# Kernel optimization log

Hardware: AMD Instinct MI355X
Metric: run time of the kernel (lower is better)

Reference implementation:

```python
import jax, jax.numpy as jnp
import numpy as np

D_MODEL = 2048
N_HEADS = 16
D_HEAD = D_MODEL // N_HEADS
B, T, CACHE_LEN = 2, 2048, 2048


def setup_inputs() -> dict:
    key = jax.random.key(0)
    k1, k2, k3, k4, k5 = jax.random.split(key, 5)
    s = 0.02
    return {
        "x": jax.random.normal(k1, (B, T, D_MODEL), dtype=jnp.float32),
        "Wqkv": jax.random.normal(k2, (3 * D_MODEL, D_MODEL), dtype=jnp.float32) * s,
        "Wproj": jax.random.normal(k3, (D_MODEL, D_MODEL), dtype=jnp.float32) * s,
        "cache_k": jax.random.normal(k4, (B, N_HEADS, CACHE_LEN, D_HEAD), dtype=jnp.float32),
        "cache_v": jax.random.normal(k5, (B, N_HEADS, CACHE_LEN, D_HEAD), dtype=jnp.float32),
    }


def reference(x, Wqkv, Wproj, cache_k, cache_v):
    b, t, c = x.shape
    h, d = N_HEADS, D_HEAD
    scale = d ** -0.5
    # qkv projection (torch Linear: x @ W.T), split into q,k,v
    qkv = jnp.einsum('btc,fc->btf', x, Wqkv)
    q, k, v = jnp.split(qkv, 3, axis=-1)
    # [b, t, c] -> [b, h, t, d]
    q = q.reshape(b, t, h, d).transpose(0, 2, 1, 3)
    k = k.reshape(b, t, h, d).transpose(0, 2, 1, 3)
    v = v.reshape(b, t, h, d).transpose(0, 2, 1, 3)
    cache_len = cache_k.shape[2]
    k = jnp.concatenate([cache_k, k], axis=2)  # [b, h, kv_len, d]
    v = jnp.concatenate([cache_v, v], axis=2)
    kv_len = k.shape[2]
    scores = jnp.einsum('bhtd,bhsd->bhts', q, k) * scale
    # causal mask with cache offset: key_pos <= query_pos
    query_pos = jnp.arange(t) + cache_len
    key_pos = jnp.arange(kv_len)
    mask = key_pos[None, :] <= query_pos[:, None]  # [t, kv_len]
    neg = jnp.finfo(scores.dtype).min
    scores = jnp.where(mask[None, None, :, :], scores, neg)
    attn = jax.nn.softmax(scores, axis=-1)
    y = jnp.einsum('bhts,bhsd->bhtd', attn, v)
    y = y.transpose(0, 2, 1, 3).reshape(b, t, c)
    return jnp.einsum('btc,oc->bto', y, Wproj)
```

## Files before the change

### kernel.cpp

```cpp
#include <hip/hip_runtime.h>

#define B_ 2
#define T_ 2048
#define H_ 16
#define D_ 128
#define DM_ 2048
#define CL_ 2048
#define KV_ 4096

typedef __attribute__((ext_vector_type(8))) short short8;
typedef __attribute__((ext_vector_type(4))) float f32x4;
typedef __attribute__((ext_vector_type(16))) float f32x16;
typedef unsigned short u16;

__device__ __forceinline__ u16 f2bf(float f) {
    unsigned u = __float_as_uint(f);
    u += 0x7FFFu + ((u >> 16) & 1u);
    return (u16)(u >> 16);
}

__device__ __forceinline__ void gload16(const void* g, void* l) {
    __builtin_amdgcn_global_load_lds((__attribute__((address_space(1))) const void*)g,
                                     (__attribute__((address_space(3))) void*)l, 16, 0, 0);
}


__global__ void cvt4(const float* __restrict__ src, u16* __restrict__ dst, int n4) {
    int i = blockIdx.x * 256 + threadIdx.x;
    if (i >= n4) return;
    const float4 v = *(const float4*)(src + (long)i * 4);
    ushort4 o;
    o.x = f2bf(v.x); o.y = f2bf(v.y); o.z = f2bf(v.z); o.w = f2bf(v.w);
    *(ushort4*)(dst + (long)i * 4) = o;
}

__global__ void cvt_cachek(const float* __restrict__ ck, u16* __restrict__ Kc) {
    int i = blockIdx.x * 256 + threadIdx.x;
    int kc = i & 15, s = (i >> 4) & 2047, bh = i >> 15;
    const float* src = ck + ((long)bh * 2048 + s) * 128 + kc * 8;
    float4 v0 = *(const float4*)src, v1 = *(const float4*)(src + 4);
    short8 o;
    o[0] = f2bf(v0.x); o[1] = f2bf(v0.y); o[2] = f2bf(v0.z); o[3] = f2bf(v0.w);
    o[4] = f2bf(v1.x); o[5] = f2bf(v1.y); o[6] = f2bf(v1.z); o[7] = f2bf(v1.w);
    *(short8*)(Kc + ((long)(bh * 16 + kc) * 4096 + s) * 8) = o;
}

__global__ void cvt_cachev(const float* __restrict__ cv, u16* __restrict__ Vc) {
    int i = blockIdx.x * 256 + threadIdx.x;
    int d = i & 127, ch = (i >> 7) & 255, bh = i >> 15;
    const float* src = cv + ((long)bh * 2048 + ch * 8) * 128 + d;
    short8 o;
#pragma unroll
    for (int j = 0; j < 8; ++j) o[j] = f2bf(src[j * 128]);
    *(short8*)(Vc + ((long)(bh * 512 + ch) * 128 + d) * 8) = o;
}


template <int MODE>
__global__ void gemm_bt(const u16* __restrict__ A, const u16* __restrict__ Bt,
                        int K,
                        u16* __restrict__ Qb, u16* __restrict__ Kc,
                        u16* __restrict__ Vc, float* __restrict__ Out) {
    __shared__ __align__(16) char A_lds[128 * 128];
    __shared__ __align__(16) char B_lds[128 * 128];

    const int tid = threadIdx.x;
    const int w = tid >> 6, l = tid & 63;
    const int wm = w >> 1, wn = w & 1;
    const int lg = l >> 4, lc = l & 15;
    const long m0 = (long)blockIdx.y * 128, n0 = (long)blockIdx.x * 128;

    f32x4 acc[4][4] = {};

    const char* Ab = (const char*)A + m0 * (K * 2);
    const char* Bb = (const char*)Bt + n0 * (K * 2);

    for (int k0 = 0; k0 < K; k0 += 64) {
#pragma unroll
        for (int j = 0; j < 4; ++j) {
            int o = ((w * 4 + j) << 10) + l * 16;
            int row = o >> 7, col = o & 127;
            gload16(Ab + (long)row * (K * 2) + k0 * 2 + col, A_lds + ((w * 4 + j) << 10));
            gload16(Bb + (long)row * (K * 2) + k0 * 2 + col, B_lds + ((w * 4 + j) << 10));
        }
        __syncthreads();
#pragma unroll
        for (int kk = 0; kk < 64; kk += 32) {
            short8 a[4], b[4];
#pragma unroll
            for (int f = 0; f < 4; ++f) {
                a[f] = *(const short8*)(A_lds + (wm * 64 + f * 16 + lc) * 128 + (kk + lg * 8) * 2);
                b[f] = *(const short8*)(B_lds + (wn * 64 + f * 16 + lc) * 128 + (kk + lg * 8) * 2);
            }
#pragma unroll
            for (int mf = 0; mf < 4; ++mf)
#pragma unroll
                for (int nf = 0; nf < 4; ++nf)
                    acc[mf][nf] = __builtin_amdgcn_mfma_f32_16x16x32_bf16(a[mf], b[nf], acc[mf][nf], 0, 0, 0);
        }
        __syncthreads();
    }

    const float qscale = 0.088388347648318447f;
#pragma unroll
    for (int mf = 0; mf < 4; ++mf) {
#pragma unroll
        for (int nf = 0; nf < 4; ++nf) {
            int mbase = (int)m0 + wm * 64 + mf * 16 + lg * 4;
            int n = (int)n0 + wn * 64 + nf * 16 + lc;
#pragma unroll
            for (int r = 0; r < 4; ++r) {
                float c = acc[mf][nf][r];
                int m = mbase + r;
                if (MODE == 0) {
                    int b = m >> 11, t = m & 2047;
                    int sec = n >> 11, f = n & 2047;
                    int h = f >> 7, d = f & 127;
                    long bh = b * H_ + h;
                    int s = CL_ + t;
                    if (sec == 0)      Qb[(bh * T_ + t) * D_ + d] = f2bf(c * qscale);
                    else if (sec == 1) Kc[((bh * 16 + (d >> 3)) * 4096L + s) * 8 + (d & 7)] = f2bf(c);
                    else               Vc[((bh * 512 + (s >> 3)) * 128L + d) * 8 + (s & 7)] = f2bf(c);
                } else {
                    Out[(long)m * DM_ + n] = c;
                }
            }
        }
    }
}


__global__ __launch_bounds__(256, 2) void attn_fwd(const u16* __restrict__ Qb,
                                                   const u16* __restrict__ Kc,
                                                   const u16* __restrict__ Vc,
                                                   u16* __restrict__ Yb) {
    __shared__ __align__(16) char Klds[2][16384];

    const int tid = threadIdx.x;
    const int w = tid >> 6, l = tid & 63;
    const int col = l & 31, half = l >> 5;
    const int blk = blockIdx.x;
    const int xcd = blk & 7, ii = blk >> 3;
    const int bh = xcd * 4 + ((ii >> 4) & 1) + (((ii >> 5) & 1) << 1);
    const int q0 = ((ii & 32) ? (15 - (ii & 15)) : (ii & 15)) << 7;
    const int qw0 = q0 + w * 32;

    const char* kcb = (const char*)Kc + (long)bh * 1048576;
    const char* vcb = (const char*)Vc + (long)bh * 1048576;

    short8 qf[8];
    const u16* qp = Qb + ((long)bh * T_ + qw0 + col) * D_ + half * 8;
#pragma unroll
    for (int kmf = 0; kmf < 8; ++kmf) qf[kmf] = *(const short8*)(qp + kmf * 16);

    f32x16 oa[4] = {};
    float mrun = -1e38f, lrun = 0.f;

    auto stageK = [&](int s0, int b) {
#pragma unroll
        for (int j = 0; j < 4; ++j) {
            int kc = w * 4 + j;
            gload16(kcb + (long)kc * 65536 + (long)(s0 + l) * 16, Klds[b] + kc * 1024);
        }
    };

    stageK(0, 0);
    __syncthreads();

    const int sLast = q0 + 2112;
    int cur = 0;
    for (int s0 = 0; s0 <= sLast; s0 += 64) {
        const bool active = (s0 <= qw0 + 31 + CL_);

        short8 vf[16];
        if (active) {
            const char* vsrc = vcb + (long)s0 * 256;
#pragma unroll
            for (int db = 0; db < 4; ++db)
#pragma unroll
                for (int smf = 0; smf < 4; ++smf)
                    vf[db * 4 + smf] =
                        *(const short8*)(vsrc + (((smf * 2 + half) * 128 + db * 32 + col) << 4));
        }

        if (s0 < sLast) stageK(s0 + 64, cur ^ 1);

        if (active) {
            f32x16 p0 = {}, p1 = {};
#pragma unroll
            for (int kmf = 0; kmf < 8; ++kmf) {
                const char* kbase = Klds[cur] + (((kmf * 2 + half) * 64 + col) << 4);
                short8 kf0 = *(const short8*)(kbase);
                short8 kf1 = *(const short8*)(kbase + (32 << 4));
                p0 = __builtin_amdgcn_mfma_f32_32x32x16_bf16(kf0, qf[kmf], p0, 0, 0, 0);
                p1 = __builtin_amdgcn_mfma_f32_32x32x16_bf16(kf1, qf[kmf], p1, 0, 0, 0);
            }

            if (s0 + 63 > qw0 + CL_) {
                int qg = qw0 + col + CL_;
#pragma unroll
                for (int r = 0; r < 16; ++r) {
                    int sl = s0 + (r & 3) + 8 * (r >> 2) + 4 * half;
                    if (sl > qg)      p0[r] = -3e38f;
                    if (sl + 32 > qg) p1[r] = -3e38f;
                }
            }

            float m8[8];
#pragma unroll
            for (int i = 0; i < 8; ++i)
                m8[i] = fmaxf(fmaxf(p0[i], p0[i + 8]), fmaxf(p1[i], p1[i + 8]));
            float pmax = fmaxf(fmaxf(fmaxf(m8[0], m8[1]), fmaxf(m8[2], m8[3])),
                               fmaxf(fmaxf(m8[4], m8[5]), fmaxf(m8[6], m8[7])));
            pmax = fmaxf(pmax, __shfl_xor(pmax, 32));

            if (!__all(pmax - mrun <= 0.0f)) {
                float mnew = fmaxf(mrun, pmax);
                float scl = __expf(mrun - mnew);
                mrun = mnew;
                lrun *= scl;
                float sc[16];
#pragma unroll
                for (int r = 0; r < 16; ++r) sc[r] = __shfl(scl, (r & 3) + 8 * (r >> 2) + 4 * half);
#pragma unroll
                for (int db = 0; db < 4; ++db)
#pragma unroll
                    for (int r = 0; r < 16; ++r) oa[db][r] *= sc[r];
            }

#pragma unroll
            for (int r = 0; r < 16; ++r) {
                p0[r] = __expf(p0[r] - mrun);
                p1[r] = __expf(p1[r] - mrun);
            }
            float s8[8];
#pragma unroll
            for (int i = 0; i < 8; ++i) s8[i] = (p0[i] + p0[i + 8]) + (p1[i] + p1[i + 8]);
            float ts = ((s8[0] + s8[1]) + (s8[2] + s8[3])) + ((s8[4] + s8[5]) + (s8[6] + s8[7]));
            lrun += ts + __shfl_xor(ts, 32);

            short8 pa[4];
#pragma unroll
            for (int smf = 0; smf < 4; ++smf) {
                const f32x16& pp = (smf < 2) ? p0 : p1;
                const int r0 = (smf & 1) * 8;
                unsigned Alo = (unsigned)f2bf(pp[r0 + 0]) | ((unsigned)f2bf(pp[r0 + 1]) << 16);
                unsigned Ahi = (unsigned)f2bf(pp[r0 + 2]) | ((unsigned)f2bf(pp[r0 + 3]) << 16);
                unsigned Blo = (unsigned)f2bf(pp[r0 + 4]) | ((unsigned)f2bf(pp[r0 + 5]) << 16);
                unsigned Bhi = (unsigned)f2bf(pp[r0 + 6]) | ((unsigned)f2bf(pp[r0 + 7]) << 16);
                unsigned sAlo = __shfl_xor(Alo, 32), sAhi = __shfl_xor(Ahi, 32);
                unsigned sBlo = __shfl_xor(Blo, 32), sBhi = __shfl_xor(Bhi, 32);
                union { unsigned u[4]; short8 s; } U;
                if (half == 0) { U.u[0] = Alo;  U.u[1] = Ahi;  U.u[2] = sAlo; U.u[3] = sAhi; }
                else           { U.u[0] = sBlo; U.u[1] = sBhi; U.u[2] = Blo;  U.u[3] = Bhi; }
                pa[smf] = U.s;
            }

#pragma unroll
            for (int db = 0; db < 4; ++db) {
#pragma unroll
                for (int smf = 0; smf < 4; ++smf)
                    oa[db] = __builtin_amdgcn_mfma_f32_32x32x16_bf16(pa[smf], vf[db * 4 + smf], oa[db], 0, 0, 0);
            }
        }

        __syncthreads();
        cur ^= 1;
    }

    float inv = 1.0f / lrun;
    float li[16];
#pragma unroll
    for (int r = 0; r < 16; ++r) li[r] = __shfl(inv, (r & 3) + 8 * (r >> 2) + 4 * half);

    const int b = bh >> 4, h = bh & 15;
#pragma unroll
    for (int db = 0; db < 4; ++db)
#pragma unroll
        for (int r = 0; r < 16; ++r) {
            int t = qw0 + (r & 3) + 8 * (r >> 2) + 4 * half;
            Yb[((long)b * T_ + t) * DM_ + h * 128 + db * 32 + col] = f2bf(oa[db][r] * li[r]);
        }
}


extern "C" void kernel_launch(void* const* d_in, const int* in_sizes, int n_in,
                              void* d_out, int out_size, void* d_ws, size_t ws_size,
                              hipStream_t stream) {
    const float* x    = (const float*)d_in[0];
    const float* Wqkv = (const float*)d_in[1];
    const float* Wpr  = (const float*)d_in[2];
    const float* cK   = (const float*)d_in[3];
    const float* cV   = (const float*)d_in[4];
    float* out = (float*)d_out;

    char* p = (char*)d_ws;
    auto take = [&](long elems) { u16* r = (u16*)p; p += ((elems * 2 + 255) & ~255L); return r; };
    u16* xb  = take((long)B_ * T_ * DM_);
    u16* wqb = take((long)3 * DM_ * DM_);
    u16* wpb = take((long)DM_ * DM_);
    u16* Qb  = take((long)B_ * H_ * T_ * D_);
    u16* Kc  = take((long)B_ * H_ * KV_ * D_);
    u16* Vc  = take((long)B_ * H_ * KV_ * D_);
    u16* Yb  = take((long)B_ * T_ * DM_);

    cvt4<<<(B_ * T_ * DM_ / 4 + 255) / 256, 256, 0, stream>>>(x, xb, B_ * T_ * DM_ / 4);
    cvt4<<<(3 * DM_ * DM_ / 4 + 255) / 256, 256, 0, stream>>>(Wqkv, wqb, 3 * DM_ * DM_ / 4);
    cvt4<<<(DM_ * DM_ / 4 + 255) / 256, 256, 0, stream>>>(Wpr, wpb, DM_ * DM_ / 4);
    cvt_cachek<<<(32 * 16 * 2048) / 256, 256, 0, stream>>>(cK, Kc);
    cvt_cachev<<<(32 * 256 * 128) / 256, 256, 0, stream>>>(cV, Vc);

    gemm_bt<0><<<dim3(48, 32), 256, 0, stream>>>(xb, wqb, 2048, Qb, Kc, Vc, nullptr);
    attn_fwd<<<512, 256, 0, stream>>>(Qb, Kc, Vc, Yb);
    gemm_bt<1><<<dim3(16, 32), 256, 0, stream>>>(Yb, wpb, 2048, nullptr, nullptr, nullptr, out);
}
```

Baseline: 522.2 us.

## Split attention into 64-query blocks of 2 waves, use exp2 and packed bf16 convert

The attention kernel now launches 1024 blocks of 128 threads, each covering 64 queries instead of 128. The block-to-(head, query) mapping is reworked to balance causal work across XCDs, and the per-wave active check is removed. The Q scale now folds in log2(e) so softmax can use exp2f, and P is converted to bf16 with the hardware v_cvt_pk_bf16_f32 instruction instead of manual rounding. Smaller blocks aim to improve load balance and the tail, but each K tile is reused by fewer queries, so K staging traffic per query doubles.

```diff
diff --git a/kernel.cpp b/kernel.cpp
--- a/kernel.cpp
+++ b/kernel.cpp
@@ -22,6 +22,12 @@
 __device__ __forceinline__ void gload16(const void* g, void* l) {
     __builtin_amdgcn_global_load_lds((__attribute__((address_space(1))) const void*)g,
                                      (__attribute__((address_space(3))) void*)l, 16, 0, 0);
+}
+
+__device__ __forceinline__ unsigned cvtpk(float a, float b) {
+    unsigned r;
+    asm("v_cvt_pk_bf16_f32 %0, %1, %2" : "=v"(r) : "v"(a), "v"(b));
+    return r;
 }
 
 
@@ -101,7 +107,7 @@
         __syncthreads();
     }
 
-    const float qscale = 0.088388347648318447f;
+    const float qscale = 0.12751743f;
 #pragma unroll
     for (int mf = 0; mf < 4; ++mf) {
 #pragma unroll
@@ -130,7 +136,7 @@
 }
 
 
-__global__ __launch_bounds__(256, 2) void attn_fwd(const u16* __restrict__ Qb,
+__global__ __launch_bounds__(128, 2) void attn_fwd(const u16* __restrict__ Qb,
                                                    const u16* __restrict__ Kc,
                                                    const u16* __restrict__ Vc,
                                                    u16* __restrict__ Yb) {
@@ -140,9 +146,13 @@
     const int w = tid >> 6, l = tid & 63;
     const int col = l & 31, half = l >> 5;
     const int blk = blockIdx.x;
-    const int xcd = blk & 7, ii = blk >> 3;
-    const int bh = xcd * 4 + ((ii >> 4) & 1) + (((ii >> 5) & 1) << 1);
-    const int q0 = ((ii & 32) ? (15 - (ii & 15)) : (ii & 15)) << 7;
+    const int xcd = blk & 7, r_ = blk >> 3;
+    const int bh = xcd * 4 + (r_ & 3);
+    const int qq = r_ >> 2;
+    const int k4 = qq & 7, j4 = qq >> 3;
+    const int qpair = (j4 == 0) ? k4 : (j4 == 1) ? (15 - k4)
+                    : (j4 == 2) ? (16 + k4) : (31 - k4);
+    const int q0 = qpair << 6;
     const int qw0 = q0 + w * 32;
 
     const char* kcb = (const char*)Kc + (long)bh * 1048576;
@@ -158,8 +168,8 @@
 
     auto stageK = [&](int s0, int b) {
 #pragma unroll
-        for (int j = 0; j < 4; ++j) {
-            int kc = w * 4 + j;
+        for (int j = 0; j < 8; ++j) {
+            int kc = w * 8 + j;
             gload16(kcb + (long)kc * 65536 + (long)(s0 + l) * 16, Klds[b] + kc * 1024);
         }
     };
@@ -167,13 +177,11 @@
     stageK(0, 0);
     __syncthreads();
 
-    const int sLast = q0 + 2112;
+    const int sLast = q0 + 2048;
     int cur = 0;
     for (int s0 = 0; s0 <= sLast; s0 += 64) {
-        const bool active = (s0 <= qw0 + 31 + CL_);
-
         short8 vf[16];
-        if (active) {
+        {
             const char* vsrc = vcb + (long)s0 * 256;
 #pragma unroll
             for (int db = 0; db < 4; ++db)
@@ -185,83 +193,81 @@
 
         if (s0 < sLast) stageK(s0 + 64, cur ^ 1);
 
-        if (active) {
-            f32x16 p0 = {}, p1 = {};
-#pragma unroll
-            for (int kmf = 0; kmf < 8; ++kmf) {
-                const char* kbase = Klds[cur] + (((kmf * 2 + half) * 64 + col) << 4);
-                short8 kf0 = *(const short8*)(kbase);
-                short8 kf1 = *(const short8*)(kbase + (32 << 4));
-                p0 = __builtin_amdgcn_mfma_f32_32x32x16_bf16(kf0, qf[kmf], p0, 0, 0, 0);
-                p1 = __builtin_amdgcn_mfma_f32_32x32x16_bf16(kf1, qf[kmf], p1, 0, 0, 0);
+        f32x16 p0 = {}, p1 = {};
+#pragma unroll
+        for (int kmf = 0; kmf < 8; ++kmf) {
+            const char* kbase = Klds[cur] + (((kmf * 2 + half) * 64 + col) << 4);
+            short8 kf0 = *(const short8*)(kbase);
+            short8 kf1 = *(const short8*)(kbase + (32 << 4));
+            p0 = __builtin_amdgcn_mfma_f32_32x32x16_bf16(kf0, qf[kmf], p0, 0, 0, 0);
+            p1 = __builtin_amdgcn_mfma_f32_32x32x16_bf16(kf1, qf[kmf], p1, 0, 0, 0);
+        }
+
+        if (s0 + 63 > qw0 + CL_) {
+            int qg = qw0 + col + CL_;
+#pragma unroll
+            for (int r = 0; r < 16; ++r) {
+                int sl = s0 + (r & 3) + 8 * (r >> 2) + 4 * half;
+                if (sl > qg)      p0[r] = -3e38f;
+                if (sl + 32 > qg) p1[r] = -3e38f;
             }
-
-            if (s0 + 63 > qw0 + CL_) {
-                int qg = qw0 + col + CL_;
-#pragma unroll
-                for (int r = 0; r < 16; ++r) {
-                    int sl = s0 + (r & 3) + 8 * (r >> 2) + 4 * half;
-                    if (sl > qg)      p0[r] = -3e38f;
-                    if (sl + 32 > qg) p1[r] = -3e38f;
-                }
-            }
-
-            float m8[8];
-#pragma unroll
-            for (int i = 0; i < 8; ++i)
-                m8[i] = fmaxf(fmaxf(p0[i], p0[i + 8]), fmaxf(p1[i], p1[i + 8]));
-            float pmax = fmaxf(fmaxf(fmaxf(m8[0], m8[1]), fmaxf(m8[2], m8[3])),
-                               fmaxf(fmaxf(m8[4], m8[5]), fmaxf(m8[6], m8[7])));
-            pmax = fmaxf(pmax, __shfl_xor(pmax, 32));
-
-            if (!__all(pmax - mrun <= 0.0f)) {
-                float mnew = fmaxf(mrun, pmax);
-                float scl = __expf(mrun - mnew);
-                mrun = mnew;
-                lrun *= scl;
-                float sc[16];
-#pragma unroll
-                for (int r = 0; r < 16; ++r) sc[r] = __shfl(scl, (r & 3) + 8 * (r >> 2) + 4 * half);
-#pragma unroll
-                for (int db = 0; db < 4; ++db)
-#pragma unroll
-                    for (int r = 0; r < 16; ++r) oa[db][r] *= sc[r];
-            }
-
-#pragma unroll
-            for (int r = 0; r < 16; ++r) {
-                p0[r] = __expf(p0[r] - mrun);
-                p1[r] = __expf(p1[r] - mrun);
-            }
-            float s8[8];
-#pragma unroll
-            for (int i = 0; i < 8; ++i) s8[i] = (p0[i] + p0[i + 8]) + (p1[i] + p1[i + 8]);
-            float ts = ((s8[0] + s8[1]) + (s8[2] + s8[3])) + ((s8[4] + s8[5]) + (s8[6] + s8[7]));
-            lrun += ts + __shfl_xor(ts, 32);
-
-            short8 pa[4];
-#pragma unroll
-            for (int smf = 0; smf < 4; ++smf) {
-                const f32x16& pp = (smf < 2) ? p0 : p1;
-                const int r0 = (smf & 1) * 8;
-                unsigned Alo = (unsigned)f2bf(pp[r0 + 0]) | ((unsigned)f2bf(pp[r0 + 1]) << 16);
-                unsigned Ahi = (unsigned)f2bf(pp[r0 + 2]) | ((unsigned)f2bf(pp[r0 + 3]) << 16);
-                unsigned Blo = (unsigned)f2bf(pp[r0 + 4]) | ((unsigned)f2bf(pp[r0 + 5]) << 16);
-                unsigned Bhi = (unsigned)f2bf(pp[r0 + 6]) | ((unsigned)f2bf(pp[r0 + 7]) << 16);
-                unsigned sAlo = __shfl_xor(Alo, 32), sAhi = __shfl_xor(Ahi, 32);
-                unsigned sBlo = __shfl_xor(Blo, 32), sBhi = __shfl_xor(Bhi, 32);
-                union { unsigned u[4]; short8 s; } U;
-                if (half == 0) { U.u[0] = Alo;  U.u[1] = Ahi;  U.u[2] = sAlo; U.u[3] = sAhi; }
-                else           { U.u[0] = sBlo; U.u[1] = sBhi; U.u[2] = Blo;  U.u[3] = Bhi; }
-                pa[smf] = U.s;
-            }
-
-#pragma unroll
-            for (int db = 0; db < 4; ++db) {
-#pragma unroll
-                for (int smf = 0; smf < 4; ++smf)
-                    oa[db] = __builtin_amdgcn_mfma_f32_32x32x16_bf16(pa[smf], vf[db * 4 + smf], oa[db], 0, 0, 0);
-            }
+        }
+
+        float m8[8];
+#pragma unroll
+        for (int i = 0; i < 8; ++i)
+            m8[i] = fmaxf(fmaxf(p0[i], p0[i + 8]), fmaxf(p1[i], p1[i + 8]));
+        float pmax = fmaxf(fmaxf(fmaxf(m8[0], m8[1]), fmaxf(m8[2], m8[3])),
+                           fmaxf(fmaxf(m8[4], m8[5]), fmaxf(m8[6], m8[7])));
+        pmax = fmaxf(pmax, __shfl_xor(pmax, 32));
+
+        if (!__all(pmax - mrun <= 0.0f)) {
+            float mnew = fmaxf(mrun, pmax);
+            float scl = exp2f(mrun - mnew);
+            mrun = mnew;
+            lrun *= scl;
+            float sc[16];
+#pragma unroll
+            for (int r = 0; r < 16; ++r) sc[r] = __shfl(scl, (r & 3) + 8 * (r >> 2) + 4 * half);
+#pragma unroll
+            for (int db = 0; db < 4; ++db)
+#pragma unroll
+                for (int r = 0; r < 16; ++r) oa[db][r] *= sc[r];
+        }
+
+#pragma unroll
+        for (int r = 0; r < 16; ++r) {
+            p0[r] = exp2f(p0[r] - mrun);
+            p1[r] = exp2f(p1[r] - mrun);
+        }
+        float s8[8];
+#pragma unroll
+        for (int i = 0; i < 8; ++i) s8[i] = (p0[i] + p0[i + 8]) + (p1[i] + p1[i + 8]);
+        float ts = ((s8[0] + s8[1]) + (s8[2] + s8[3])) + ((s8[4] + s8[5]) + (s8[6] + s8[7]));
+        lrun += ts + __shfl_xor(ts, 32);
+
+        short8 pa[4];
+#pragma unroll
+        for (int smf = 0; smf < 4; ++smf) {
+            const f32x16& pp = (smf < 2) ? p0 : p1;
+            const int r0 = (smf & 1) * 8;
+            unsigned Alo = cvtpk(pp[r0 + 0], pp[r0 + 1]);
+            unsigned Ahi = cvtpk(pp[r0 + 2], pp[r0 + 3]);
+            unsigned Blo = cvtpk(pp[r0 + 4], pp[r0 + 5]);
+            unsigned Bhi = cvtpk(pp[r0 + 6], pp[r0 + 7]);
+            unsigned sAlo = __shfl_xor(Alo, 32), sAhi = __shfl_xor(Ahi, 32);
+            unsigned sBlo = __shfl_xor(Blo, 32), sBhi = __shfl_xor(Bhi, 32);
+            union { unsigned u[4]; short8 s; } U;
+            if (half == 0) { U.u[0] = Alo;  U.u[1] = Ahi;  U.u[2] = sAlo; U.u[3] = sAhi; }
+            else           { U.u[0] = sBlo; U.u[1] = sBhi; U.u[2] = Blo;  U.u[3] = Bhi; }
+            pa[smf] = U.s;
+        }
+
+#pragma unroll
+        for (int db = 0; db < 4; ++db) {
+#pragma unroll
+            for (int smf = 0; smf < 4; ++smf)
+                oa[db] = __builtin_amdgcn_mfma_f32_32x32x16_bf16(pa[smf], vf[db * 4 + smf], oa[db], 0, 0, 0);
         }
 
         __syncthreads();
@@ -311,6 +317,6 @@
     cvt_cachev<<<(32 * 256 * 128) / 256, 256, 0, stream>>>(cV, Vc);
 
     gemm_bt<0><<<dim3(48, 32), 256, 0, stream>>>(xb, wqb, 2048, Qb, Kc, Vc, nullptr);
-    attn_fwd<<<512, 256, 0, stream>>>(Qb, Kc, Vc, Yb);
+    attn_fwd<<<1024, 128, 0, stream>>>(Qb, Kc, Vc, Yb);
     gemm_bt<1><<<dim3(16, 32), 256, 0, stream>>>(Yb, wpb, 2048, nullptr, nullptr, nullptr, out);
 }
```

New measurement: 540.9 us. 3.6% more time.

## Remap GEMM blocks per XCD, use exp2 softmax and packed bf16 conversion

Applied to the files above, without the earlier changes.

GEMM launches become 1D, with block indices remapped so each XCD handles a contiguous group of N tiles, improving L2 reuse of weight tiles. The Q scale folds in log2(e) so attention softmax can use exp2 instead of exp. Manual float-to-bf16 rounding of probabilities is replaced with the hardware packed conversion instruction. These reduce ALU work in the attention inner loop and cache misses in the GEMMs, at the cost of dependence on the XCD dispatch order assumption.

```diff
diff --git a/kernel.cpp b/kernel.cpp
--- a/kernel.cpp
+++ b/kernel.cpp
@@ -22,6 +22,12 @@
 __device__ __forceinline__ void gload16(const void* g, void* l) {
     __builtin_amdgcn_global_load_lds((__attribute__((address_space(1))) const void*)g,
                                      (__attribute__((address_space(3))) void*)l, 16, 0, 0);
+}
+
+__device__ __forceinline__ unsigned cvtpk(float a, float b) {
+    unsigned r;
+    asm("v_cvt_pk_bf16_f32 %0, %1, %2" : "=v"(r) : "v"(a), "v"(b));
+    return r;
 }
 
 
@@ -68,7 +74,15 @@
     const int w = tid >> 6, l = tid & 63;
     const int wm = w >> 1, wn = w & 1;
     const int lg = l >> 4, lc = l & 15;
-    const long m0 = (long)blockIdx.y * 128, n0 = (long)blockIdx.x * 128;
+
+    const int blk = blockIdx.x;
+    const int xcd = blk & 7;
+    const int b2 = blk >> 3;
+    const int mt = b2 & 31;
+    const int nl = b2 >> 5;
+    const int NT = (MODE == 0) ? 6 : 2;
+    const long m0 = (long)mt * 128;
+    const long n0 = (long)(xcd * NT + nl) * 128;
 
     f32x4 acc[4][4] = {};
 
@@ -101,7 +115,7 @@
         __syncthreads();
     }
 
-    const float qscale = 0.088388347648318447f;
+    const float qscale = 0.12751743f;
 #pragma unroll
     for (int mf = 0; mf < 4; ++mf) {
 #pragma unroll
@@ -216,7 +230,7 @@
 
             if (!__all(pmax - mrun <= 0.0f)) {
                 float mnew = fmaxf(mrun, pmax);
-                float scl = __expf(mrun - mnew);
+                float scl = exp2f(mrun - mnew);
                 mrun = mnew;
                 lrun *= scl;
                 float sc[16];
@@ -230,8 +244,8 @@
 
 #pragma unroll
             for (int r = 0; r < 16; ++r) {
-                p0[r] = __expf(p0[r] - mrun);
-                p1[r] = __expf(p1[r] - mrun);
+                p0[r] = exp2f(p0[r] - mrun);
+                p1[r] = exp2f(p1[r] - mrun);
             }
             float s8[8];
 #pragma unroll
@@ -244,10 +258,10 @@
             for (int smf = 0; smf < 4; ++smf) {
                 const f32x16& pp = (smf < 2) ? p0 : p1;
                 const int r0 = (smf & 1) * 8;
-                unsigned Alo = (unsigned)f2bf(pp[r0 + 0]) | ((unsigned)f2bf(pp[r0 + 1]) << 16);
-                unsigned Ahi = (unsigned)f2bf(pp[r0 + 2]) | ((unsigned)f2bf(pp[r0 + 3]) << 16);
-                unsigned Blo = (unsigned)f2bf(pp[r0 + 4]) | ((unsigned)f2bf(pp[r0 + 5]) << 16);
-                unsigned Bhi = (unsigned)f2bf(pp[r0 + 6]) | ((unsigned)f2bf(pp[r0 + 7]) << 16);
+                unsigned Alo = cvtpk(pp[r0 + 0], pp[r0 + 1]);
+                unsigned Ahi = cvtpk(pp[r0 + 2], pp[r0 + 3]);
+                unsigned Blo = cvtpk(pp[r0 + 4], pp[r0 + 5]);
+                unsigned Bhi = cvtpk(pp[r0 + 6], pp[r0 + 7]);
                 unsigned sAlo = __shfl_xor(Alo, 32), sAhi = __shfl_xor(Ahi, 32);
                 unsigned sBlo = __shfl_xor(Blo, 32), sBhi = __shfl_xor(Bhi, 32);
                 union { unsigned u[4]; short8 s; } U;
@@ -310,7 +324,7 @@
     cvt_cachek<<<(32 * 16 * 2048) / 256, 256, 0, stream>>>(cK, Kc);
     cvt_cachev<<<(32 * 256 * 128) / 256, 256, 0, stream>>>(cV, Vc);
 
-    gemm_bt<0><<<dim3(48, 32), 256, 0, stream>>>(xb, wqb, 2048, Qb, Kc, Vc, nullptr);
+    gemm_bt<0><<<1536, 256, 0, stream>>>(xb, wqb, 2048, Qb, Kc, Vc, nullptr);
     attn_fwd<<<512, 256, 0, stream>>>(Qb, Kc, Vc, Yb);
-    gemm_bt<1><<<dim3(16, 32), 256, 0, stream>>>(Yb, wpb, 2048, nullptr, nullptr, nullptr, out);
-}
+    gemm_bt<1><<<512, 256, 0, stream>>>(Yb, wpb, 2048, nullptr, nullptr, nullptr, out);
+}
```

After: 549.8 us. +5.3%, slower.
